# Performance work log

Measured on AMD Instinct MI355X. Metric: run time of the kernel, lower is better.

The kernel has to match this reference:

```python
import jax, jax.numpy as jnp
import numpy as np

B, S, D, H = 2, 2048, 1024, 16
DK = D // H

def setup_inputs() -> dict:
    key = jax.random.key(0)
    ks = jax.random.split(key, 11)
    sc = 1.0 / np.sqrt(D)
    return {
        "q": jax.random.normal(ks[0], (B, S, D), jnp.float32),
        "k": jax.random.normal(ks[1], (B, S, D), jnp.float32),
        "v": jax.random.normal(ks[2], (B, S, D), jnp.float32),
        "Wq": jax.random.normal(ks[3], (D, D), jnp.float32) * sc,
        "bq": jax.random.normal(ks[4], (D,), jnp.float32) * sc,
        "Wk": jax.random.normal(ks[5], (D, D), jnp.float32) * sc,
        "bk": jax.random.normal(ks[6], (D,), jnp.float32) * sc,
        "Wv": jax.random.normal(ks[7], (D, D), jnp.float32) * sc,
        "bv": jax.random.normal(ks[8], (D,), jnp.float32) * sc,
        "Wo": jax.random.normal(ks[9], (D, D), jnp.float32) * sc,
        "bo": jax.random.normal(ks[10], (D,), jnp.float32) * sc,
    }

def reference(q, k, v, Wq, bq, Wk, bk, Wv, bv, Wo, bo):
    b, s, d = q.shape
    # projections (torch Linear: x @ W^T + b)
    qh = (q @ Wq.T + bq).reshape(b, s, H, DK).transpose(0, 2, 1, 3)  # [B,H,S,DK]
    kh = (k @ Wk.T + bk).reshape(b, s, H, DK).transpose(0, 2, 1, 3)
    vh = (v @ Wv.T + bv).reshape(b, s, H, DK).transpose(0, 2, 1, 3)
    scores = jnp.einsum('bhqd,bhkd->bhqk', qh, kh) / jnp.sqrt(jnp.float32(DK))
    attn = jax.nn.softmax(scores, axis=-1)  # [B,H,S,S]
    out = jnp.einsum('bhqk,bhkd->bhqd', attn, vh)  # [B,H,S,DK]
    out = out.transpose(0, 2, 1, 3).reshape(b, s, d)
    return out @ Wo.T + bo
```

## Files before the change

### kernel.cpp

```cpp
#include <hip/hip_runtime.h>
#include <hip/hip_bf16.h>
#include <stdint.h>

typedef __bf16 bf16;
typedef __attribute__((ext_vector_type(8))) __bf16 bf16x8;
typedef __attribute__((ext_vector_type(4))) float f32x4;
typedef __attribute__((ext_vector_type(16))) float f32x16;
typedef __attribute__((ext_vector_type(4))) unsigned int u32x4;
typedef __attribute__((ext_vector_type(2))) unsigned int u32x2;

#define BATCH  2
#define SEQ    2048
#define DMODEL 1024
#define NH     16
#define DKH    64
#define BS     (BATCH*SEQ)
#define BSD    (BS*DMODEL)
#define DD     (DMODEL*DMODEL)

#define QSCALE 0.18033688f

__device__ __forceinline__ void gload_lds16(const bf16* g, bf16* l) {
  __builtin_amdgcn_global_load_lds((const __attribute__((address_space(1))) void*)g,
                                   (__attribute__((address_space(3))) void*)l,
                                   16, 0, 0);
}

__device__ __forceinline__ unsigned int packbf2(float a, float b) {
  union { bf16 h[2]; unsigned int u; } z;
  z.h[0] = (bf16)a; z.h[1] = (bf16)b;
  return z.u;
}

__device__ __forceinline__ float exp2_raw(float x) {
  float r;
  asm("v_exp_f32 %0, %1" : "=v"(r) : "v"(x));
  return r;
}

__global__ __launch_bounds__(256) void cvtW_kernel(
    const float* __restrict__ a, const float* __restrict__ b,
    const float* __restrict__ c, const float* __restrict__ d,
    bf16* __restrict__ oa, bf16* __restrict__ ob,
    bf16* __restrict__ oc, bf16* __restrict__ od) {
  int i = blockIdx.x * blockDim.x + threadIdx.x;
  const int z = blockIdx.y;
  const float* in = (z == 0) ? a : (z == 1) ? b : (z == 2) ? c : d;
  bf16* out       = (z == 0) ? oa : (z == 1) ? ob : (z == 2) ? oc : od;
  const f32x4* p = (const f32x4*)in + (size_t)i * 2;
  f32x4 x = p[0], y = p[1];
  bf16x8 o;
  o[0]=(bf16)x[0]; o[1]=(bf16)x[1]; o[2]=(bf16)x[2]; o[3]=(bf16)x[3];
  o[4]=(bf16)y[0]; o[5]=(bf16)y[1]; o[6]=(bf16)y[2]; o[7]=(bf16)y[3];
  ((bf16x8*)out)[i] = o;
}

template <typename OUT, int MODE, int MR, typename AT>
__device__ __forceinline__ void gemm_body(const AT* __restrict__ A,
                                          const bf16* __restrict__ W,
                                          const float* __restrict__ bias,
                                          OUT* __restrict__ C,
                                          float oscale,
                                          bf16* Als, bf16* Bls,
                                          int tx, int ty) {
  constexpr bool AF32 = (sizeof(AT) == 4);
  const int tid  = threadIdx.x;
  const int lane = tid & 63;
  const int wave = tid >> 6;
  const int wm = wave >> 1, wn = wave & 1;
  const int c = lane & 15, g = lane >> 4;
  const long brow = (long)ty * (MR * 32);
  const long bcol = (long)tx * 128;
  const int  N = DMODEL, K = DMODEL;
  const int  ABUF = MR * 1024;

  f32x4 acc[MR][4] = {};

  const AT*   Ag = A + (brow + wave*16 + ((lane>>2)&15)) * (long)K + (lane & 3) * 8;
  const bf16* Bg = W + (bcol + wave*16 + ((lane>>2)&15)) * (long)K + (lane & 3) * 8;

  f32x4 ar[2][2];

  auto stage_issue = [&](int kt, int buf) {
    if constexpr (AF32) {
      const float* a0 = (const float*)Ag + kt * 32;
      ar[0][0] = *(const f32x4*)a0;
      ar[0][1] = *(const f32x4*)(a0 + 4);
      const float* a1 = a0 + 64 * (long)K;
      ar[1][0] = *(const f32x4*)a1;
      ar[1][1] = *(const f32x4*)(a1 + 4);
    } else {
      const bf16* a0 = (const bf16*)Ag + kt * 32;
      bf16* Ad = Als + buf * ABUF + wave * 512;
      gload_lds16(a0, Ad);
      if (MR == 4) gload_lds16(a0 + 64 * (long)K, Ad + 2048);
    }
    const bf16* b0 = Bg + kt * 32;
    bf16* Bd = Bls + buf * 4096 + wave * 512;
    gload_lds16(b0, Bd);
    gload_lds16(b0 + 64 * (long)K, Bd + 2048);
  };
  auto stage_writeA = [&](int buf) {
    if constexpr (AF32) {
      bf16* Ad = Als + buf * ABUF + wave * 512 + lane * 8;
      #pragma unroll
      for (int u = 0; u < 2; ++u) {
        u32x4 pk;
        pk[0] = packbf2(ar[u][0][0], ar[u][0][1]);
        pk[1] = packbf2(ar[u][0][2], ar[u][0][3]);
        pk[2] = packbf2(ar[u][1][0], ar[u][1][1]);
        pk[3] = packbf2(ar[u][1][2], ar[u][1][3]);
        *(u32x4*)(Ad + u * 2048) = pk;
      }
    }
  };

  const int nk = K >> 5;
  stage_issue(0, 0);
  stage_writeA(0);
  int cur = 0;
  for (int kt = 0; kt < nk; ++kt) {
    __syncthreads();
    if (kt + 1 < nk) stage_issue(kt + 1, cur ^ 1);

    bf16x8 af[MR], bfv[4];
    #pragma unroll
    for (int m = 0; m < MR; ++m)
      af[m] = *(const bf16x8*)(Als + cur * ABUF + (wm*(MR*16) + m*16 + c) * 32 + g * 8);
    #pragma unroll
    for (int n = 0; n < 4; ++n)
      bfv[n] = *(const bf16x8*)(Bls + cur * 4096 + (wn*64 + n*16 + c) * 32 + g * 8);
    __builtin_amdgcn_s_setprio(1);
    #pragma unroll
    for (int m = 0; m < MR; ++m)
      #pragma unroll
      for (int n = 0; n < 4; ++n)
        acc[m][n] = __builtin_amdgcn_mfma_f32_16x16x32_bf16(af[m], bfv[n], acc[m][n], 0, 0, 0);
    __builtin_amdgcn_s_setprio(0);
    if (kt + 1 < nk) stage_writeA(cur ^ 1);
    cur ^= 1;
  }

  if (MODE == 0) {
    #pragma unroll
    for (int n = 0; n < 4; ++n) {
      const long col = bcol + wn*64 + n*16 + c;
      const float bb = bias[col];
      #pragma unroll
      for (int m = 0; m < MR; ++m) {
        #pragma unroll
        for (int r = 0; r < 4; ++r) {
          const long row = brow + wm*(MR*16) + m*16 + g*4 + r;
          C[row * (long)N + col] = (OUT)((acc[m][n][r] + bb) * oscale);
        }
      }
    }
  } else {
    const int srow = (int)(brow & (SEQ - 1));
    const int bidx = (int)(brow >> 11);
    #pragma unroll
    for (int n = 0; n < 4; ++n) {
      const int col = (int)bcol + wn*64 + n*16 + c;
      const float bb = bias[col];
      const int h = col >> 6, dk = col & 63;
      OUT* rowp = C + ((size_t)((bidx*16 + h)*64 + dk)) * SEQ + srow + wm*64;
      #pragma unroll
      for (int m = 0; m < MR; ++m) {
        u32x2 pkd;
        pkd[0] = packbf2(acc[m][n][0] + bb, acc[m][n][1] + bb);
        pkd[1] = packbf2(acc[m][n][2] + bb, acc[m][n][3] + bb);
        *(u32x2*)(rowp + m*16 + g*4) = pkd;
      }
    }
  }
}

__global__ __launch_bounds__(256) void gemm_qkv_kernel(
    const float* __restrict__ q, const float* __restrict__ k, const float* __restrict__ v,
    const bf16* __restrict__ Wqb, const bf16* __restrict__ Wkb, const bf16* __restrict__ Wvb,
    const float* __restrict__ bq, const float* __restrict__ bk, const float* __restrict__ bv,
    bf16* __restrict__ qh, bf16* __restrict__ kh, bf16* __restrict__ vt) {
  __shared__ bf16 Als[2 * 128 * 32];
  __shared__ bf16 Bls[2 * 128 * 32];
  const int bid  = blockIdx.x + (blockIdx.y << 3) + (blockIdx.z << 8);
  const int tile = (bid & 7) * 96 + (bid >> 3);
  const int tx = tile & 7, ty = (tile >> 3) & 31, tz = tile >> 8;
  if (tz == 2) {
    gemm_body<bf16, 1, 4, float>(v, Wvb, bv, vt, 1.0f, Als, Bls, tx, ty);
  } else {
    const float* A  = (tz == 0) ? q   : k;
    const bf16*  W  = (tz == 0) ? Wqb : Wkb;
    const float* bi = (tz == 0) ? bq  : bk;
    bf16*        Cp = (tz == 0) ? qh  : kh;
    const float  os = (tz == 0) ? QSCALE : 1.0f;
    gemm_body<bf16, 0, 4, float>(A, W, bi, Cp, os, Als, Bls, tx, ty);
  }
}

__global__ __launch_bounds__(256) void gemm_out_kernel(
    const bf16* __restrict__ A, const bf16* __restrict__ Wob,
    const float* __restrict__ bo, float* __restrict__ C) {
  __shared__ bf16 Als[2 * 64 * 32];
  __shared__ bf16 Bls[2 * 128 * 32];
  const int bid  = blockIdx.x + (blockIdx.y << 3);
  const int tile = (bid & 7) * 64 + (bid >> 3);
  const int tx = tile & 7, ty = tile >> 3;
  gemm_body<float, 0, 2, bf16>(A, Wob, bo, C, 1.0f, Als, Bls, tx, ty);
}

__global__ __launch_bounds__(512) void attn_kernel(const bf16* __restrict__ qh,
                                                   const bf16* __restrict__ kh,
                                                   const bf16* __restrict__ vt,
                                                   bf16* __restrict__ ao) {
  __shared__ char smem[65536];
  bf16* Kbase = (bf16*)smem;
  bf16* Vbase = (bf16*)(smem + 32768);

  const int tid = threadIdx.x;
  const int lane = tid & 63, wave = tid >> 6;
  const int q32 = lane & 31, hi = lane >> 5;
  const int qg = wave >> 1, half = wave & 1;

  const int bx  = blockIdx.x;
  const int bh  = (bx & 7) * 4 + ((bx >> 3) >> 4);
  const int qt  = (bx >> 3) & 15;
  const int b = bh >> 4, h = bh & 15;
  const long rowbase = (long)b * SEQ;
  const int q0 = qt * 128 + qg * 32;

  const bf16* qp = qh + (rowbase + q0 + q32) * DMODEL + h * 64 + hi * 8;
  bf16x8 qf[4];
  #pragma unroll
  for (int ks = 0; ks < 4; ++ks) qf[ks] = *(const bf16x8*)(qp + ks * 16);

  f32x16 accO0 = {}, accO1 = {};
  f32x16 accL  = {};

  bf16x8 ones8;
  {
    const bf16 sel = (q32 == 0) ? (bf16)1.0f : (bf16)0.0f;
    #pragma unroll
    for (int j = 0; j < 8; ++j) ones8[j] = sel;
  }

  int rd[2][4];
  #pragma unroll
  for (int hh = 0; hh < 2; ++hh) {
    const int row = q32 + 32 * hh;
    const int sw = (row & 7) << 4;
    #pragma unroll
    for (int ks = 0; ks < 4; ++ks)
      rd[hh][ks] = row * 128 + ((ks * 32 + hi * 16) ^ sw);
  }

  const int st_half = tid >> 8;
  const int t8 = tid & 255;
  const int srw = t8 >> 3, stc = t8 & 7;
  const int soff = srw * 128 + ((stc * 16) ^ ((srw & 7) << 4));
  u32x4 kreg0, kreg1, vreg0, vreg1;

  const bf16* kp = kh + (rowbase + st_half * 1024 + srw) * DMODEL + h * 64 + stc * 8;
  const bf16* vp = vt + ((size_t)bh * 64 + srw) * SEQ + st_half * 1024 + stc * 8;

  auto load_tiles = [&]() {
    kreg0 = *(const u32x4*)kp;
    kreg1 = *(const u32x4*)(kp + 32 * DMODEL);
    vreg0 = *(const u32x4*)vp;
    vreg1 = *(const u32x4*)(vp + 32 * SEQ);
    kp += 64 * DMODEL;
    vp += 64;
  };
  auto write_tiles = [&](int buf) {
    char* Kb = (char*)(Kbase + (buf * 2 + st_half) * 4096);
    char* Vb = (char*)(Vbase + (buf * 2 + st_half) * 4096);
    *(u32x4*)(Kb + soff)        = kreg0;
    *(u32x4*)(Kb + soff + 4096) = kreg1;
    *(u32x4*)(Vb + soff)        = vreg0;
    *(u32x4*)(Vb + soff + 4096) = vreg1;
  };

  load_tiles();
  write_tiles(0);
  int cur = 0;
  const int NT2 = SEQ / 64 / 2;

  for (int t = 0; t < NT2; ++t) {
    __syncthreads();
    if (t + 1 < NT2) load_tiles();

    const char* Kb = (const char*)(Kbase + (cur * 2 + half) * 4096);
    const char* Vb = (const char*)(Vbase + (cur * 2 + half) * 4096);

    f32x16 s0 = {}, s1 = {};
    __builtin_amdgcn_s_setprio(1);
    #pragma unroll
    for (int ks = 0; ks < 4; ++ks) {
      bf16x8 k0 = *(const bf16x8*)(Kb + rd[0][ks]);
      s0 = __builtin_amdgcn_mfma_f32_32x32x16_bf16(k0, qf[ks], s0, 0, 0, 0);
    }
    #pragma unroll
    for (int ks = 0; ks < 4; ++ks) {
      bf16x8 k1 = *(const bf16x8*)(Kb + rd[1][ks]);
      s1 = __builtin_amdgcn_mfma_f32_32x32x16_bf16(k1, qf[ks], s1, 0, 0, 0);
    }
    __builtin_amdgcn_s_setprio(0);

    unsigned W0[4][2], W1[4][2];
    #pragma unroll
    for (int t4 = 0; t4 < 4; ++t4) {
      float a0 = exp2_raw(s0[4*t4+0]), a1 = exp2_raw(s0[4*t4+1]);
      float a2 = exp2_raw(s0[4*t4+2]), a3 = exp2_raw(s0[4*t4+3]);
      W0[t4][0] = packbf2(a0, a1); W0[t4][1] = packbf2(a2, a3);
      float b0 = exp2_raw(s1[4*t4+0]), b1 = exp2_raw(s1[4*t4+1]);
      float b2 = exp2_raw(s1[4*t4+2]), b3 = exp2_raw(s1[4*t4+3]);
      W1[t4][0] = packbf2(b0, b1); W1[t4][1] = packbf2(b2, b3);
    }

    bf16x8 Pb[4];
    #pragma unroll
    for (int ks = 0; ks < 4; ++ks) {
      const int t0 = 2 * (ks & 1);
      unsigned w0 = (ks < 2) ? W0[t0][0]     : W1[t0][0];
      unsigned w2 = (ks < 2) ? W0[t0 + 1][0] : W1[t0 + 1][0];
      unsigned w1 = (ks < 2) ? W0[t0][1]     : W1[t0][1];
      unsigned w3 = (ks < 2) ? W0[t0 + 1][1] : W1[t0 + 1][1];
      asm("v_permlane32_swap_b32 %0, %1" : "+v"(w0), "+v"(w2));
      asm("v_permlane32_swap_b32 %0, %1" : "+v"(w1), "+v"(w3));
      union { unsigned u[4]; bf16x8 v; } P;
      P.u[0] = w0; P.u[1] = w1; P.u[2] = w2; P.u[3] = w3;
      Pb[ks] = P.v;
    }

    __builtin_amdgcn_s_setprio(1);
    #pragma unroll
    for (int ks = 0; ks < 4; ++ks) {
      bf16x8 v0 = *(const bf16x8*)(Vb + rd[0][ks]);
      accO0 = __builtin_amdgcn_mfma_f32_32x32x16_bf16(v0, Pb[ks], accO0, 0, 0, 0);
    }
    #pragma unroll
    for (int ks = 0; ks < 4; ++ks) {
      bf16x8 v1 = *(const bf16x8*)(Vb + rd[1][ks]);
      accO1 = __builtin_amdgcn_mfma_f32_32x32x16_bf16(v1, Pb[ks], accO1, 0, 0, 0);
    }
    #pragma unroll
    for (int ks = 0; ks < 4; ++ks)
      accL = __builtin_amdgcn_mfma_f32_32x32x16_bf16(ones8, Pb[ks], accL, 0, 0, 0);
    __builtin_amdgcn_s_setprio(0);

    if (t + 1 < NT2) write_tiles(cur ^ 1);
    cur ^= 1;
  }

  const float lpart = __shfl(accL[0], q32);
  __syncthreads();
  float* cb = (float*)smem + qg * 2176;
  if (half == 1) {
    #pragma unroll
    for (int i = 0; i < 16; ++i) {
      cb[lane + 64 * i]        = accO0[i];
      cb[lane + 64 * (16 + i)] = accO1[i];
    }
    cb[lane + 64 * 32] = lpart;
  }
  __syncthreads();
  if (half == 0) {
    const float lall = lpart + cb[lane + 64 * 32];
    const float inv = 1.f / lall;
    #pragma unroll
    for (int i = 0; i < 16; ++i) {
      accO0[i] += cb[lane + 64 * i];
      accO1[i] += cb[lane + 64 * (16 + i)];
    }
    bf16* dst = ao + (rowbase + q0 + q32) * DMODEL + h * 64;
    #pragma unroll
    for (int t4 = 0; t4 < 4; ++t4) {
      const int d0 = 8 * t4 + 4 * hi;
      u32x2 p0, p1;
      p0[0] = packbf2(accO0[4*t4+0] * inv, accO0[4*t4+1] * inv);
      p0[1] = packbf2(accO0[4*t4+2] * inv, accO0[4*t4+3] * inv);
      *(u32x2*)(dst + d0) = p0;
      p1[0] = packbf2(accO1[4*t4+0] * inv, accO1[4*t4+1] * inv);
      p1[1] = packbf2(accO1[4*t4+2] * inv, accO1[4*t4+3] * inv);
      *(u32x2*)(dst + d0 + 32) = p1;
    }
  }
}

extern "C" void kernel_launch(void* const* d_in, const int* in_sizes, int n_in,
                              void* d_out, int out_size, void* d_ws, size_t ws_size,
                              hipStream_t stream) {
  const float* q  = (const float*)d_in[0];
  const float* k  = (const float*)d_in[1];
  const float* v  = (const float*)d_in[2];
  const float* Wq = (const float*)d_in[3];
  const float* bq = (const float*)d_in[4];
  const float* Wk = (const float*)d_in[5];
  const float* bk = (const float*)d_in[6];
  const float* Wv = (const float*)d_in[7];
  const float* bv = (const float*)d_in[8];
  const float* Wo = (const float*)d_in[9];
  const float* bo = (const float*)d_in[10];
  float* out = (float*)d_out;

  char* w = (char*)d_ws;
  bf16* Wqb = (bf16*)w; w += (size_t)DD * 2;
  bf16* Wkb = (bf16*)w; w += (size_t)DD * 2;
  bf16* Wvb = (bf16*)w; w += (size_t)DD * 2;
  bf16* Wob = (bf16*)w; w += (size_t)DD * 2;
  bf16* qhd = (bf16*)w; w += (size_t)BSD * 2;
  bf16* khd = (bf16*)w; w += (size_t)BSD * 2;
  bf16* vtd = (bf16*)w; w += (size_t)BSD * 2;
  bf16* aod = (bf16*)w; w += (size_t)BSD * 2;

  cvtW_kernel<<<dim3(DD / 8 / 256, 4), 256, 0, stream>>>(
      Wq, Wk, Wv, Wo, Wqb, Wkb, Wvb, Wob);

  gemm_qkv_kernel<<<dim3(8, 32, 3), 256, 0, stream>>>(q, k, v, Wqb, Wkb, Wvb,
                                                      bq, bk, bv, qhd, khd, vtd);
  attn_kernel<<<512, 512, 0, stream>>>(qhd, khd, vtd, aod);
  gemm_out_kernel<<<dim3(8, 64), 256, 0, stream>>>(aod, Wob, bo, out);
}
```

Before: 120.2 us.

## Halve QKV GEMM M-tile and deepen fp32 A prefetch to two stages

Result: slower. 133.1 us (+10.7%).

```diff
diff --git a/kernel.cpp b/kernel.cpp
--- a/kernel.cpp
+++ b/kernel.cpp
@@ -76,53 +76,17 @@
 
   f32x4 acc[MR][4] = {};
 
-  const AT*   Ag = A + (brow + wave*16 + ((lane>>2)&15)) * (long)K + (lane & 3) * 8;
-  const bf16* Bg = W + (bcol + wave*16 + ((lane>>2)&15)) * (long)K + (lane & 3) * 8;
-
-  f32x4 ar[2][2];
-
-  auto stage_issue = [&](int kt, int buf) {
-    if constexpr (AF32) {
-      const float* a0 = (const float*)Ag + kt * 32;
-      ar[0][0] = *(const f32x4*)a0;
-      ar[0][1] = *(const f32x4*)(a0 + 4);
-      const float* a1 = a0 + 64 * (long)K;
-      ar[1][0] = *(const f32x4*)a1;
-      ar[1][1] = *(const f32x4*)(a1 + 4);
-    } else {
-      const bf16* a0 = (const bf16*)Ag + kt * 32;
-      bf16* Ad = Als + buf * ABUF + wave * 512;
-      gload_lds16(a0, Ad);
-      if (MR == 4) gload_lds16(a0 + 64 * (long)K, Ad + 2048);
-    }
+  const AT*   Ag = A + (brow + wave*16 + (lane>>2)) * (long)K + (lane & 3) * 8;
+  const bf16* Bg = W + (bcol + wave*16 + (lane>>2)) * (long)K + (lane & 3) * 8;
+
+  auto issueB = [&](int kt, int buf) {
     const bf16* b0 = Bg + kt * 32;
     bf16* Bd = Bls + buf * 4096 + wave * 512;
     gload_lds16(b0, Bd);
     gload_lds16(b0 + 64 * (long)K, Bd + 2048);
   };
-  auto stage_writeA = [&](int buf) {
-    if constexpr (AF32) {
-      bf16* Ad = Als + buf * ABUF + wave * 512 + lane * 8;
-      #pragma unroll
-      for (int u = 0; u < 2; ++u) {
-        u32x4 pk;
-        pk[0] = packbf2(ar[u][0][0], ar[u][0][1]);
-        pk[1] = packbf2(ar[u][0][2], ar[u][0][3]);
-        pk[2] = packbf2(ar[u][1][0], ar[u][1][1]);
-        pk[3] = packbf2(ar[u][1][2], ar[u][1][3]);
-        *(u32x4*)(Ad + u * 2048) = pk;
-      }
-    }
-  };
-
-  const int nk = K >> 5;
-  stage_issue(0, 0);
-  stage_writeA(0);
-  int cur = 0;
-  for (int kt = 0; kt < nk; ++kt) {
-    __syncthreads();
-    if (kt + 1 < nk) stage_issue(kt + 1, cur ^ 1);
-
+
+  auto compute = [&](int cur) {
     bf16x8 af[MR], bfv[4];
     #pragma unroll
     for (int m = 0; m < MR; ++m)
@@ -137,8 +101,63 @@
       for (int n = 0; n < 4; ++n)
         acc[m][n] = __builtin_amdgcn_mfma_f32_16x16x32_bf16(af[m], bfv[n], acc[m][n], 0, 0, 0);
     __builtin_amdgcn_s_setprio(0);
-    if (kt + 1 < nk) stage_writeA(cur ^ 1);
-    cur ^= 1;
+  };
+
+  const int nk = K >> 5;
+
+  if constexpr (AF32) {
+    static_assert(MR == 2, "fp32 A staging geometry assumes BM=64");
+    f32x4 arA[2], arB[2];
+    auto loadA = [&](f32x4* ar, int kt) {
+      const float* a0 = (const float*)Ag + kt * 32;
+      ar[0] = *(const f32x4*)a0;
+      ar[1] = *(const f32x4*)(a0 + 4);
+    };
+    auto writeA = [&](const f32x4* ar, int buf) {
+      bf16* Ad = Als + buf * ABUF + wave * 512 + lane * 8;
+      u32x4 pk;
+      pk[0] = packbf2(ar[0][0], ar[0][1]);
+      pk[1] = packbf2(ar[0][2], ar[0][3]);
+      pk[2] = packbf2(ar[1][0], ar[1][1]);
+      pk[3] = packbf2(ar[1][2], ar[1][3]);
+      *(u32x4*)Ad = pk;
+    };
+
+    loadA(arA, 0);
+    writeA(arA, 0);
+    issueB(0, 0);
+    loadA(arB, 1);
+    int cur = 0;
+    for (int kt = 0; kt < nk; kt += 2) {
+      __syncthreads();
+      if (kt + 1 < nk) issueB(kt + 1, cur ^ 1);
+      if (kt + 2 < nk) loadA(arA, kt + 2);
+      compute(cur);
+      if (kt + 1 < nk) writeA(arB, cur ^ 1);
+      cur ^= 1;
+      __syncthreads();
+      if (kt + 2 < nk) issueB(kt + 2, cur ^ 1);
+      if (kt + 3 < nk) loadA(arB, kt + 3);
+      compute(cur);
+      if (kt + 2 < nk) writeA(arA, cur ^ 1);
+      cur ^= 1;
+    }
+  } else {
+    auto stage = [&](int kt, int buf) {
+      const bf16* a0 = (const bf16*)Ag + kt * 32;
+      bf16* Ad = Als + buf * ABUF + wave * 512;
+      gload_lds16(a0, Ad);
+      if (MR == 4) gload_lds16(a0 + 64 * (long)K, Ad + 2048);
+      issueB(kt, buf);
+    };
+    stage(0, 0);
+    int cur = 0;
+    for (int kt = 0; kt < nk; ++kt) {
+      __syncthreads();
+      if (kt + 1 < nk) stage(kt + 1, cur ^ 1);
+      compute(cur);
+      cur ^= 1;
+    }
   }
 
   if (MODE == 0) {
@@ -163,7 +182,7 @@
       const int col = (int)bcol + wn*64 + n*16 + c;
       const float bb = bias[col];
       const int h = col >> 6, dk = col & 63;
-      OUT* rowp = C + ((size_t)((bidx*16 + h)*64 + dk)) * SEQ + srow + wm*64;
+      OUT* rowp = C + ((size_t)((bidx*16 + h)*64 + dk)) * SEQ + srow + wm*(MR*16);
       #pragma unroll
       for (int m = 0; m < MR; ++m) {
         u32x2 pkd;
@@ -180,20 +199,20 @@
     const bf16* __restrict__ Wqb, const bf16* __restrict__ Wkb, const bf16* __restrict__ Wvb,
     const float* __restrict__ bq, const float* __restrict__ bk, const float* __restrict__ bv,
     bf16* __restrict__ qh, bf16* __restrict__ kh, bf16* __restrict__ vt) {
-  __shared__ bf16 Als[2 * 128 * 32];
+  __shared__ bf16 Als[2 * 64 * 32];
   __shared__ bf16 Bls[2 * 128 * 32];
-  const int bid  = blockIdx.x + (blockIdx.y << 3) + (blockIdx.z << 8);
-  const int tile = (bid & 7) * 96 + (bid >> 3);
-  const int tx = tile & 7, ty = (tile >> 3) & 31, tz = tile >> 8;
+  const int bid  = blockIdx.x + (blockIdx.y << 3) + (blockIdx.z << 9);
+  const int tile = (bid & 7) * 192 + (bid >> 3);
+  const int tx = tile & 7, ty = (tile >> 3) & 63, tz = tile >> 9;
   if (tz == 2) {
-    gemm_body<bf16, 1, 4, float>(v, Wvb, bv, vt, 1.0f, Als, Bls, tx, ty);
+    gemm_body<bf16, 1, 2, float>(v, Wvb, bv, vt, 1.0f, Als, Bls, tx, ty);
   } else {
     const float* A  = (tz == 0) ? q   : k;
     const bf16*  W  = (tz == 0) ? Wqb : Wkb;
     const float* bi = (tz == 0) ? bq  : bk;
     bf16*        Cp = (tz == 0) ? qh  : kh;
     const float  os = (tz == 0) ? QSCALE : 1.0f;
-    gemm_body<bf16, 0, 4, float>(A, W, bi, Cp, os, Als, Bls, tx, ty);
+    gemm_body<bf16, 0, 2, float>(A, W, bi, Cp, os, Als, Bls, tx, ty);
   }
 }
 
@@ -415,7 +434,7 @@
   cvtW_kernel<<<dim3(DD / 8 / 256, 4), 256, 0, stream>>>(
       Wq, Wk, Wv, Wo, Wqb, Wkb, Wvb, Wob);
 
-  gemm_qkv_kernel<<<dim3(8, 32, 3), 256, 0, stream>>>(q, k, v, Wqb, Wkb, Wvb,
+  gemm_qkv_kernel<<<dim3(8, 64, 3), 256, 0, stream>>>(q, k, v, Wqb, Wkb, Wvb,
                                                       bq, bk, bv, qhd, khd, vtd);
   attn_kernel<<<512, 512, 0, stream>>>(qhd, khd, vtd, aod);
   gemm_out_kernel<<<dim3(8, 64), 256, 0, stream>>>(aod, Wob, bo, out);
```
